# Performance work log

Hardware: AMD Instinct MI355X
Metric: run time of the kernel (lower is better)

## Reference

```python
import jax, jax.numpy as jnp
import numpy as np

DECAY = 0.99
EPS = 1e-05
THRESHOLD = 2.0
CODEBOOK_SIZE = 2048
DIM = 256


def setup_inputs() -> dict:
    key = jax.random.key(0)
    k1, k2, k3 = jax.random.split(key, 3)
    x = jax.random.normal(k1, (32, 1500, DIM), dtype=jnp.float32)
    # kaiming_uniform_ with a=0: bound = sqrt(6 / fan_in)
    bound = float(np.sqrt(6.0 / DIM))
    embed = jax.random.uniform(k2, (CODEBOOK_SIZE, DIM), dtype=jnp.float32,
                               minval=-bound, maxval=bound)
    # warm EMA state: positive cluster sizes, consistent embed_avg
    cluster_size = jax.random.uniform(k3, (CODEBOOK_SIZE,), dtype=jnp.float32,
                                      minval=0.0, maxval=200.0)
    embed_avg = embed * cluster_size[:, None]
    return {"x": x, "embed": embed, "cluster_size": cluster_size,
            "embed_avg": embed_avg}


def reference(x, embed, cluster_size, embed_avg):
    shape = x.shape
    K = embed.shape[0]
    xf = x.reshape(-1, shape[-1])                       # [N, D]

    # quantize: negative squared Euclidean distance, argmax == argmin dist
    x2 = jnp.sum(xf * xf, axis=1, keepdims=True)        # [N, 1]
    e2 = jnp.sum(embed * embed, axis=1)                 # [K]
    dist = -(x2 - 2.0 * (xf @ embed.T) + e2[None, :])   # [N, K]
    embed_ind = jnp.argmax(dist, axis=-1)               # [N]

    # dequantize (embedding gather)
    quantize = embed[embed_ind].reshape(shape)          # [B, T, D]

    # training-path EMA statistics (onehot.sum(0) and x.T @ onehot, as segment sums)
    counts = jax.ops.segment_sum(jnp.ones(xf.shape[0], dtype=x.dtype),
                                 embed_ind, num_segments=K)        # [K]
    embed_sum = jax.ops.segment_sum(xf, embed_ind, num_segments=K) # [K, D]

    new_cluster_size = cluster_size * DECAY + (1.0 - DECAY) * counts
    new_embed_avg = embed_avg * DECAY + (1.0 - DECAY) * embed_sum

    n = new_cluster_size.sum()
    smoothed = (new_cluster_size + EPS) / (n + K * EPS) * n
    embed_normalized = new_embed_avg / smoothed[:, None]

    # dead-code expiration: replace expired codes with random batch vectors
    expired = new_cluster_size < THRESHOLD
    perm = jax.random.permutation(jax.random.key(1), xf.shape[0])[:K]
    replacement = xf[perm]                              # [K, D]
    new_embed = jnp.where(expired[:, None], replacement, embed_normalized)

    codes = embed_ind.reshape(shape[:-1])               # [B, T]
    return quantize, codes, new_cluster_size, new_embed_avg, new_embed
```

## Files before the change

### kernel.cpp

```cpp
#include <hip/hip_runtime.h>
#include <hip/hip_bf16.h>
#include <stdint.h>
#include <math.h>

#define N_TOK 48000
#define DIMS  256
#define KCB   2048
#define WND 0.10f
#define BIAS 32.0f

typedef __attribute__((ext_vector_type(8))) short bf16x8;
typedef __attribute__((ext_vector_type(4))) float f32x4;
typedef __attribute__((ext_vector_type(8))) unsigned short u16x8;

__device__ __forceinline__ unsigned short bf16rn(float f) {
  uint32_t u = __float_as_uint(f);
  uint32_t r = (u + 0x7FFFu + ((u >> 16) & 1u)) >> 16;
  return (unsigned short)r;
}

__device__ __forceinline__ uint32_t packBiased(float fb, uint32_t invIdx) {
  float c = fmaxf(fb, 0.0f);
  return (__float_as_uint(c) & ~0x7FFu) | invIdx;
}
__device__ __forceinline__ uint32_t packThrBiased(float fb) {
  float c = fmaxf(fb, 0.0f);
  return __float_as_uint(c) & ~0x7FFu;
}
__device__ __forceinline__ float unpackBiased(uint32_t u) {
  return __uint_as_float(u & ~0x7FFu);
}
__device__ __forceinline__ void ins3u(uint32_t& b, uint32_t& s, uint32_t& t, uint32_t v) {
  uint32_t lo = min(b, v);
  b = max(b, v);
  uint32_t lo2 = min(s, lo);
  s = max(s, lo);
  t = max(t, lo2);
}

__device__ inline void tf2x32(uint32_t k0, uint32_t k1, uint32_t c0, uint32_t c1,
                              uint32_t& o0, uint32_t& o1) {
  uint32_t ks2 = k0 ^ k1 ^ 0x1BD11BDAu;
  uint32_t x0 = c0 + k0, x1 = c1 + k1;
#define TF_R(r) { x0 += x1; x1 = (x1 << (r)) | (x1 >> (32 - (r))); x1 ^= x0; }
  TF_R(13) TF_R(15) TF_R(26) TF_R(6)
  x0 += k1; x1 += ks2 + 1u;
  TF_R(17) TF_R(29) TF_R(16) TF_R(24)
  x0 += ks2; x1 += k0 + 2u;
  TF_R(13) TF_R(15) TF_R(26) TF_R(6)
  x0 += k0; x1 += k1 + 3u;
  TF_R(17) TF_R(29) TF_R(16) TF_R(24)
  x0 += k1; x1 += ks2 + 4u;
  TF_R(13) TF_R(15) TF_R(26) TF_R(6)
  x0 += ks2; x1 += k0 + 5u;
#undef TF_R
  o0 = x0; o1 = x1;
}

__device__ inline void get_round_key(int round, uint32_t& ka, uint32_t& kb) {
  const uint32_t b0 = 0u, b1 = 1u;
  uint32_t K1a, K1b, S1a, S1b;
  tf2x32(b0, b1, 0u, 0u, K1a, K1b);
  tf2x32(b0, b1, 0u, 1u, S1a, S1b);
  if (round == 1) { ka = S1a; kb = S1b; return; }
  uint32_t S2a, S2b;
  tf2x32(K1a, K1b, 0u, 1u, S2a, S2b);
  ka = S2a; kb = S2b;
}

__device__ inline uint32_t gen_key(int round, uint32_t i) {
  uint32_t ka, kb, o0, o1;
  get_round_key(round, ka, kb);
  tf2x32(ka, kb, 0u, i, o0, o1);
  return o0 ^ o1;
}

__device__ __forceinline__ void gload_lds16(const void* g, void* l) {
  __builtin_amdgcn_global_load_lds(
      (const __attribute__((address_space(1))) uint32_t*)g,
      (__attribute__((address_space(3))) uint32_t*)l, 16, 0, 0);
}

__global__ void e2split(const float* __restrict__ x, unsigned short* __restrict__ xh,
                        const float* __restrict__ embed, unsigned short* __restrict__ eh,
                        float* __restrict__ e2f, double* __restrict__ e2d) {
  const int nx = N_TOK * DIMS / 8;
  const int ne = KCB * DIMS / 8;
  int i = blockIdx.x * blockDim.x + threadIdx.x;
  if (i < nx + ne) {
    const float* src; unsigned short* dst; int j;
    if (i < nx) { src = x; dst = xh; j = i; }
    else { src = embed; dst = eh; j = i - nx; }
    float4 a = ((const float4*)src)[j * 2];
    float4 b = ((const float4*)src)[j * 2 + 1];
    float v[8] = {a.x, a.y, a.z, a.w, b.x, b.y, b.z, b.w};
    u16x8 h;
#pragma unroll
    for (int q = 0; q < 8; ++q) h[q] = bf16rn(v[q]);
    *(u16x8*)&dst[(size_t)j * 8] = h;
    return;
  }
  int k = i - (nx + ne);
  if (k < KCB) {
    const float4* er = (const float4*)(embed + (size_t)k * DIMS);
    float s = 0.f;
    double sd = 0.0;
    for (int c = 0; c < DIMS / 4; ++c) {
      float4 v = er[c];
      s = fmaf(v.x, v.x, s); s = fmaf(v.y, v.y, s);
      s = fmaf(v.z, v.z, s); s = fmaf(v.w, v.w, s);
      sd += (double)v.x * v.x + (double)v.y * v.y
          + (double)v.z * v.z + (double)v.w * v.w;
    }
    e2f[k] = BIAS - s;
    e2d[k] = sd;
  }
}

__global__ __launch_bounds__(256, 2) void dist_mfma(
    const unsigned short* __restrict__ xh, const unsigned short* __restrict__ eh,
    const float* __restrict__ e2f,
    uint32_t* __restrict__ pb, uint32_t* __restrict__ ps, uint32_t* __restrict__ pt)
{
  __shared__ __align__(16) char smem[50688];
  short (*As)[128 * 32] = (short(*)[128 * 32])smem;
  short (*Bs)[256 * 32] = (short(*)[256 * 32])(smem + 16384);
  uint32_t* red = (uint32_t*)smem;

  const int tid = threadIdx.x;
  const int lane = tid & 63, w = tid >> 6;
  const int wr = w >> 1, wc = w & 1;
  const int l15 = lane & 15, lg = lane >> 4;

  int bx, by;
  {
    const int bid = blockIdx.x;
    if (bid < 2944) { int g = bid >> 6, r = bid & 63; bx = g * 8 + (r & 7); by = r >> 3; }
    else            { int t2 = bid - 2944; bx = 368 + (t2 % 7); by = t2 / 7; }
  }
  const int n0 = bx * 128;
  const int c0 = by * 256;

  f32x4 acc[4][8];
#pragma unroll
  for (int mf = 0; mf < 4; ++mf)
#pragma unroll
    for (int nf = 0; nf < 8; ++nf) acc[mf][nf] = (f32x4){0.f, 0.f, 0.f, 0.f};

  auto stage = [&](int t) {
    const int d0 = t << 5;
    const int q = t & 1;
#pragma unroll
    for (int i = 0; i < 2; ++i) {
      const int c = i * 256 + tid;
      const int row = c >> 2;
      const int sc = ((c & 3) ^ ((row >> 1) & 3)) << 3;
      gload_lds16(xh + (size_t)(n0 + row) * DIMS + d0 + sc, (void*)&As[q][c * 8]);
    }
#pragma unroll
    for (int i = 0; i < 4; ++i) {
      const int c = i * 256 + tid;
      const int row = c >> 2;
      const int sc = ((c & 3) ^ ((row >> 1) & 3)) << 3;
      gload_lds16(eh + (size_t)(c0 + row) * DIMS + d0 + sc, (void*)&Bs[q][c * 8]);
    }
  };

  stage(0);
  __syncthreads();

#pragma unroll 1
  for (int t = 0; t < 8; ++t) {
    if (t < 7) stage(t + 1);
    const int q = t & 1;
    bf16x8 af[4], bfv[8];
#pragma unroll
    for (int mf = 0; mf < 4; ++mf) {
      const int r = wr * 64 + mf * 16 + l15;
      af[mf] = *(const bf16x8*)&As[q][r * 32 + ((lg ^ ((r >> 1) & 3)) << 3)];
    }
#pragma unroll
    for (int nf = 0; nf < 8; ++nf) {
      const int r = wc * 128 + nf * 16 + l15;
      bfv[nf] = *(const bf16x8*)&Bs[q][r * 32 + ((lg ^ ((r >> 1) & 3)) << 3)];
    }
#pragma unroll
    for (int mf = 0; mf < 4; ++mf)
#pragma unroll
      for (int nf = 0; nf < 8; ++nf)
        acc[mf][nf] = __builtin_amdgcn_mfma_f32_16x16x32_bf16(
            af[mf], bfv[nf], acc[mf][nf], 0, 0, 0);
    __syncthreads();
  }

  float e2v[8];
  uint32_t inv[8];
#pragma unroll
  for (int nf = 0; nf < 8; ++nf) {
    int k = c0 + wc * 128 + nf * 16 + l15;
    e2v[nf] = e2f[k];
    inv[nf] = 2047u - (uint32_t)k;
  }

  const int colbase = wc * 16 + l15;
#pragma unroll
  for (int mf = 0; mf < 4; ++mf) {
#pragma unroll
    for (int reg = 0; reg < 4; ++reg) {
      uint32_t p0 = packBiased(fmaf(2.f, acc[mf][0][reg], e2v[0]), inv[0]);
      uint32_t p1 = packBiased(fmaf(2.f, acc[mf][1][reg], e2v[1]), inv[1]);
      uint32_t p2 = packBiased(fmaf(2.f, acc[mf][2][reg], e2v[2]), inv[2]);
      uint32_t h1 = max(p0, p1), l1 = min(p0, p1);
      uint32_t b  = max(h1, p2), m  = min(h1, p2);
      uint32_t s  = max(l1, m),  t3 = min(l1, m);
#pragma unroll
      for (int nf = 3; nf < 8; ++nf) {
        float f = fmaf(2.f, acc[mf][nf][reg], e2v[nf]);
        ins3u(b, s, t3, packBiased(f, inv[nf]));
      }
      const int row = wr * 64 + mf * 16 + lg * 4 + reg;
      uint32_t* p = &red[row * 99 + colbase * 3];
      p[0] = b; p[1] = s; p[2] = t3;
    }
  }
  __syncthreads();
  {
    const int row = tid >> 1, half = tid & 1;
    uint32_t b = 0u, s = 0u, t3 = 0u;
    const uint32_t* p = &red[row * 99 + half * 48];
#pragma unroll 4
    for (int c = 0; c < 48; ++c) ins3u(b, s, t3, p[c]);
    if (half) {
      uint32_t* q = &red[row * 99 + 96];
      q[0] = b; q[1] = s; q[2] = t3;
    }
    __syncthreads();
    if (!half) {
      const uint32_t* q = &red[row * 99 + 96];
      ins3u(b, s, t3, q[0]);
      ins3u(b, s, t3, q[1]);
      ins3u(b, s, t3, q[2]);
      size_t o = (size_t)by * N_TOK + n0 + row;
      pb[o] = b; ps[o] = s; pt[o] = t3;
    }
  }
}

__global__ void merge8(const uint32_t* __restrict__ pb, const uint32_t* __restrict__ ps,
                       const uint32_t* __restrict__ pt,
                       int* __restrict__ ind,
                       int* __restrict__ candRows, int* __restrict__ candIdx,
                       int* __restrict__ candCnt, int* __restrict__ listC,
                       uint32_t* __restrict__ cntA, uint32_t* __restrict__ cntC) {
  int n = blockIdx.x * blockDim.x + threadIdx.x;
  if (n >= N_TOK) return;
  uint32_t tb[8], tsv[8], ttv[8];
#pragma unroll
  for (int tt = 0; tt < 8; ++tt) {
    size_t o = (size_t)tt * N_TOK + n;
    tb[tt] = pb[o]; tsv[tt] = ps[o]; ttv[tt] = pt[o];
  }
  uint32_t best = tb[0];
#pragma unroll
  for (int tt = 1; tt < 8; ++tt) best = max(best, tb[tt]);
  ind[n] = 2047 - (int)(best & 0x7FFu);
  const uint32_t thr = packThrBiased(unpackBiased(best) - WND);
  int m = 0; bool full = false;
#pragma unroll
  for (int tt = 0; tt < 8; ++tt) {
    m += (tb[tt] >= thr) + (tsv[tt] >= thr);
    full = full || (ttv[tt] >= thr);
  }
  if (full) {
    listC[atomicAdd(cntC, 1u)] = n;
  } else if (m > 1) {
    uint32_t i = atomicAdd(cntA, 1u);
    candRows[i] = n; candCnt[i] = m;
    int j = 0;
#pragma unroll
    for (int tt = 0; tt < 8; ++tt) {
      if (tb[tt]  >= thr) candIdx[(size_t)i * 16 + (j++)] = 2047 - (int)(tb[tt]  & 0x7FFu);
      if (tsv[tt] >= thr) candIdx[(size_t)i * 16 + (j++)] = 2047 - (int)(tsv[tt] & 0x7FFu);
    }
  }
}

__global__ void refine_cand(const float* __restrict__ x, const float* __restrict__ embed,
                            const double* __restrict__ e2d,
                            const int* __restrict__ candRows, const int* __restrict__ candIdx,
                            const int* __restrict__ candCnt, const uint32_t* __restrict__ cntA,
                            int* __restrict__ ind) {
  const uint32_t nA = cntA[0];
  const int lane = threadIdx.x & 63;
  const uint32_t wid = (blockIdx.x * blockDim.x + threadIdx.x) >> 6;
  const uint32_t nw = (gridDim.x * blockDim.x) >> 6;
  for (uint32_t i = wid; i < nA; i += nw) {
    const int n = candRows[i];
    const int m = candCnt[i];
    float4 xv = ((const float4*)x)[(size_t)n * 64 + lane];
    double best = -1e300; int bk = 0x7fffffff;
    for (int j = 0; j < m; ++j) {
      int k = candIdx[(size_t)i * 16 + j];
      float4 e4 = ((const float4*)embed)[(size_t)k * 64 + lane];
      double d = (double)xv.x * e4.x + (double)xv.y * e4.y
               + (double)xv.z * e4.z + (double)xv.w * e4.w;
#pragma unroll
      for (int mm = 1; mm < 64; mm <<= 1) d += __shfl_xor(d, mm);
      double v = 2.0 * d - e2d[k];
      if (v > best || (v == best && k < bk)) { best = v; bk = k; }
    }
    if (lane == 0) ind[n] = bk;
  }
}

__global__ void refine_fullC(const float* __restrict__ x, const float* __restrict__ embed,
                             const double* __restrict__ e2d,
                             const int* __restrict__ listC, const uint32_t* __restrict__ cntC,
                             int* __restrict__ ind) {
  __shared__ double xd[DIMS];
  __shared__ double rv[256];
  __shared__ int    rk[256];
  const int tid = threadIdx.x;
  const uint32_t nC = cntC[0];
  for (uint32_t it = blockIdx.x; it < nC; it += gridDim.x) {
    const int n = listC[it];
    __syncthreads();
    xd[tid] = (double)x[(size_t)n * DIMS + tid];
    __syncthreads();
    double best = -1e300; int bk = 0x7fffffff;
    for (int k = tid; k < KCB; k += 256) {
      const float4* er = (const float4*)(embed + (size_t)k * DIMS);
      double a0 = 0.0, a1 = 0.0, a2 = 0.0, a3 = 0.0;
      for (int c = 0; c < 64; c += 4) {
        float4 ea = er[c], eb = er[c + 1], ec = er[c + 2], ed = er[c + 3];
        int d = c * 4;
        a0 += xd[d + 0] * ea.x + xd[d + 1] * ea.y + xd[d + 2] * ea.z + xd[d + 3] * ea.w;
        a1 += xd[d + 4] * eb.x + xd[d + 5] * eb.y + xd[d + 6] * eb.z + xd[d + 7] * eb.w;
        a2 += xd[d + 8] * ec.x + xd[d + 9] * ec.y + xd[d + 10] * ec.z + xd[d + 11] * ec.w;
        a3 += xd[d + 12] * ed.x + xd[d + 13] * ed.y + xd[d + 14] * ed.z + xd[d + 15] * ed.w;
      }
      double v = 2.0 * (a0 + a1 + a2 + a3) - e2d[k];
      if (v > best || (v == best && k < bk)) { best = v; bk = k; }
    }
    rv[tid] = best; rk[tid] = bk;
    __syncthreads();
    for (int s = 128; s > 0; s >>= 1) {
      if (tid < s) {
        double v2 = rv[tid + s]; int k2 = rk[tid + s];
        if (v2 > rv[tid] || (v2 == rv[tid] && k2 < rk[tid])) { rv[tid] = v2; rk[tid] = k2; }
      }
      __syncthreads();
    }
    if (tid == 0) ind[n] = rk[0];
  }
}

__global__ void gather_q(const float* __restrict__ embed, const int* __restrict__ ind,
                         float* __restrict__ outq, float* __restrict__ outcodes,
                         uint32_t* __restrict__ cntTok) {
  int idx = blockIdx.x * blockDim.x + threadIdx.x;
  if (idx >= N_TOK * 64) return;
  int n = idx >> 6, c = idx & 63;
  int k = ind[n];
  ((float4*)outq)[idx] = ((const float4*)embed)[(size_t)k * 64 + c];
  if (c == 0) { outcodes[n] = (float)k; atomicAdd(&cntTok[k], 1u); }
}

__global__ void scan_tok_ema(const uint32_t* __restrict__ cntTok, uint32_t* __restrict__ tokBase,
                             uint32_t* __restrict__ tokCur,
                             const float* __restrict__ cs, float* __restrict__ out_ncs,
                             int* __restrict__ expired, double* __restrict__ nsum) {
  __shared__ uint32_t buf[2][2048];
  __shared__ double sd[1024];
  int t = threadIdx.x;
  double local = 0.0;
  for (int q = 0; q < 2; ++q) {
    int i = t + q * 1024;
    uint32_t c = cntTok[i];
    buf[0][i] = c;
    tokCur[i] = 0;
    double v = 0.99 * (double)cs[i] + 0.01 * (double)c;
    out_ncs[i] = (float)v;
    expired[i] = (v < 2.0) ? 1 : 0;
    local += v;
  }
  sd[t] = local;
  __syncthreads();
  int src = 0;
  for (int off = 1; off < 2048; off <<= 1) {
    for (int q = 0; q < 2; ++q) {
      int i = t + q * 1024;
      uint32_t v = buf[src][i];
      if (i >= off) v += buf[src][i - off];
      buf[src ^ 1][i] = v;
    }
    src ^= 1; __syncthreads();
  }
  for (int q = 0; q < 2; ++q) {
    int i = t + q * 1024;
    tokBase[i] = buf[src][i] - cntTok[i];
  }
  for (int s = 512; s > 0; s >>= 1) { if (t < s) sd[t] += sd[t + s]; __syncthreads(); }
  if (t == 0) nsum[0] = sd[0];
}

__global__ void scatter_tok(const int* __restrict__ ind, const uint32_t* __restrict__ tokBase,
                            uint32_t* __restrict__ cursor, uint32_t* __restrict__ tokBucket) {
  int n = blockIdx.x * blockDim.x + threadIdx.x;
  if (n >= N_TOK) return;
  int k = ind[n];
  uint32_t p = atomicAdd(&cursor[k], 1u);
  tokBucket[tokBase[k] + p] = (uint32_t)n;
}

__global__ void esum_bucket(const float* __restrict__ x, const uint32_t* __restrict__ tokBase,
                            const uint32_t* __restrict__ cntTok,
                            const uint32_t* __restrict__ tokBucket,
                            float* __restrict__ esum) {
  const uint32_t wv = (blockIdx.x * blockDim.x + threadIdx.x) >> 6;
  if (wv >= KCB) return;
  const int lane = threadIdx.x & 63;
  const uint32_t base = tokBase[wv], cnt = cntTok[wv];
  float4 a0 = {0.f, 0.f, 0.f, 0.f}, a1 = {0.f, 0.f, 0.f, 0.f};
  uint32_t i = 0;
  for (; i + 2 <= cnt; i += 2) {
    uint32_t n0 = tokBucket[base + i], n1 = tokBucket[base + i + 1];
    float4 v0 = ((const float4*)x)[(size_t)n0 * 64 + lane];
    float4 v1 = ((const float4*)x)[(size_t)n1 * 64 + lane];
    a0.x += v0.x; a0.y += v0.y; a0.z += v0.z; a0.w += v0.w;
    a1.x += v1.x; a1.y += v1.y; a1.z += v1.z; a1.w += v1.w;
  }
  if (i < cnt) {
    uint32_t n0 = tokBucket[base + i];
    float4 v0 = ((const float4*)x)[(size_t)n0 * 64 + lane];
    a0.x += v0.x; a0.y += v0.y; a0.z += v0.z; a0.w += v0.w;
  }
  float4 r; r.x = a0.x + a1.x; r.y = a0.y + a1.y; r.z = a0.z + a1.z; r.w = a0.w + a1.w;
  ((float4*)esum)[(size_t)wv * 64 + lane] = r;
}

__global__ void final_embed(const float* __restrict__ x, const float* __restrict__ cs,
                            const uint32_t* __restrict__ cntTok,
                            const float* __restrict__ eavg, const float* __restrict__ esum,
                            const int* __restrict__ expired, const double* __restrict__ nsum,
                            const uint32_t* __restrict__ perm,
                            float* __restrict__ out_eavg, float* __restrict__ out_ne) {
  int idx = blockIdx.x * blockDim.x + threadIdx.x;
  if (idx >= KCB * 64) return;
  int k = idx >> 6, c = idx & 63;
  float4 ea = ((const float4*)eavg)[idx];
  float4 es = ((const float4*)esum)[idx];
  double ax = 0.99 * (double)ea.x + 0.01 * (double)es.x;
  double ay = 0.99 * (double)ea.y + 0.01 * (double)es.y;
  double az = 0.99 * (double)ea.z + 0.01 * (double)es.z;
  double aw = 0.99 * (double)ea.w + 0.01 * (double)es.w;
  float4 nv; nv.x = (float)ax; nv.y = (float)ay; nv.z = (float)az; nv.w = (float)aw;
  ((float4*)out_eavg)[idx] = nv;
  float4 r;
  if (expired[k]) {
    r = ((const float4*)x)[(size_t)perm[k] * 64 + c];
  } else {
    double ncs = 0.99 * (double)cs[k] + 0.01 * (double)cntTok[k];
    double n = nsum[0];
    double sm = (ncs + 1e-5) / (n + 2048.0 * 1e-5) * n;
    r.x = (float)(ax / sm); r.y = (float)(ay / sm);
    r.z = (float)(az / sm); r.w = (float)(aw / sm);
  }
  ((float4*)out_ne)[idx] = r;
}

__global__ void keys_both(uint32_t* __restrict__ keys1, uint32_t* __restrict__ keys2,
                          uint32_t* __restrict__ bcount1, uint32_t* __restrict__ bcount2) {
  int i = blockIdx.x * blockDim.x + threadIdx.x;
  if (i >= N_TOK) return;
  uint32_t k1 = gen_key(1, (uint32_t)i);
  uint32_t k2 = gen_key(2, (uint32_t)i);
  keys1[i] = k1; keys2[i] = k2;
  atomicAdd(&bcount1[k1 >> 21], 1u);
  atomicAdd(&bcount2[k2 >> 21], 1u);
}

__global__ void scan_both(const uint32_t* __restrict__ in1, uint32_t* __restrict__ out1,
                          uint32_t* __restrict__ cur1,
                          const uint32_t* __restrict__ in2, uint32_t* __restrict__ out2,
                          uint32_t* __restrict__ cur2) {
  const uint32_t* in = blockIdx.x ? in2 : in1;
  uint32_t* out = blockIdx.x ? out2 : out1;
  uint32_t* cz = blockIdx.x ? cur2 : cur1;
  __shared__ uint32_t buf[2][2048];
  int t = threadIdx.x;
  for (int q = 0; q < 2; ++q) buf[0][t + q * 1024] = in[t + q * 1024];
  cz[t] = 0; cz[t + 1024] = 0;
  __syncthreads();
  int src = 0;
  for (int off = 1; off < 2048; off <<= 1) {
    for (int q = 0; q < 2; ++q) {
      int i = t + q * 1024;
      uint32_t v = buf[src][i];
      if (i >= off) v += buf[src][i - off];
      buf[src ^ 1][i] = v;
    }
    src ^= 1; __syncthreads();
  }
  for (int q = 0; q < 2; ++q) {
    int i = t + q * 1024;
    out[i] = buf[src][i] - in[i];
  }
}

__global__ void scatter1(const uint32_t* __restrict__ keys1, const uint32_t* __restrict__ bbase1,
                         uint32_t* __restrict__ cursor1,
                         uint32_t* __restrict__ bkey, uint32_t* __restrict__ bval) {
  int i = blockIdx.x * blockDim.x + threadIdx.x;
  if (i >= N_TOK) return;
  uint32_t k = keys1[i];
  uint32_t b = k >> 21;
  uint32_t p = atomicAdd(&cursor1[b], 1u);
  uint32_t s = bbase1[b] + p;
  bkey[s] = k; bval[s] = (uint32_t)i;
}

__global__ void rank1_scatter2(const uint32_t* __restrict__ bkey, const uint32_t* __restrict__ bval,
                               const uint32_t* __restrict__ bbase1, const uint32_t* __restrict__ bcount1,
                               const uint32_t* __restrict__ keys2,
                               const uint32_t* __restrict__ bbase2, uint32_t* __restrict__ cursor2,
                               uint32_t* __restrict__ bkey2, uint32_t* __restrict__ bval2,
                               uint32_t* __restrict__ bpos2) {
  int b = blockIdx.x;
  uint32_t base = bbase1[b], cnt = bcount1[b];
  for (uint32_t t = threadIdx.x; t < cnt; t += blockDim.x) {
    uint32_t k = bkey[base + t], pv = bval[base + t];
    uint32_t r = 0;
    for (uint32_t j = 0; j < cnt; ++j) {
      uint32_t kj = bkey[base + j], pj = bval[base + j];
      r += (kj < k) | ((kj == k) & (pj < pv));
    }
    uint32_t p = base + r;
    uint32_t k2 = keys2[p];
    uint32_t b2 = k2 >> 21;
    uint32_t q = atomicAdd(&cursor2[b2], 1u);
    uint32_t s = bbase2[b2] + q;
    bkey2[s] = k2; bval2[s] = pv; bpos2[s] = p;
  }
}

__global__ void rank2(const uint32_t* __restrict__ bkey2, const uint32_t* __restrict__ bval2,
                      const uint32_t* __restrict__ bpos2,
                      const uint32_t* __restrict__ bbase2, const uint32_t* __restrict__ bcount2,
                      uint32_t* __restrict__ perm) {
  int b = blockIdx.x;
  uint32_t base = bbase2[b];
  if (base >= KCB) return;
  uint32_t cnt = bcount2[b];
  for (uint32_t t = threadIdx.x; t < cnt; t += blockDim.x) {
    uint32_t k = bkey2[base + t], p = bpos2[base + t];
    uint32_t r = 0;
    for (uint32_t j = 0; j < cnt; ++j) {
      uint32_t kj = bkey2[base + j], pj = bpos2[base + j];
      r += (kj < k) | ((kj == k) & (pj < p));
    }
    uint32_t pos = base + r;
    if (pos < KCB) perm[pos] = bval2[base + t];
  }
}

extern "C" void kernel_launch(void* const* d_in, const int* in_sizes, int n_in,
                              void* d_out, int out_size, void* d_ws, size_t ws_size,
                              hipStream_t stream) {
  const float* x     = (const float*)d_in[0];
  const float* embed = (const float*)d_in[1];
  const float* cs    = (const float*)d_in[2];
  const float* eavg  = (const float*)d_in[3];

  float* out = (float*)d_out;
  float* outQ    = out;
  float* outC    = out + 12288000;
  float* outNCS  = out + 12336000;
  float* outEAVG = out + 12338048;
  float* outNE   = out + 12862336;

  char* w = (char*)d_ws;
  size_t off = 0;
  auto alloc = [&](size_t bytes) -> void* {
    void* p = w + off; off += (bytes + 255) & ~(size_t)255; return p;
  };
  unsigned short* xh = (unsigned short*)alloc((size_t)N_TOK * DIMS * 2);
  unsigned short* eh = (unsigned short*)alloc((size_t)KCB * DIMS * 2);
  float*    e2f     = (float*)alloc(KCB * 4);
  double*   e2d     = (double*)alloc(KCB * 8);
  float*    esum    = (float*)alloc((size_t)KCB * DIMS * 4);
  uint32_t* pbest   = (uint32_t*)alloc((size_t)8 * N_TOK * 4);
  uint32_t* psecond = (uint32_t*)alloc((size_t)8 * N_TOK * 4);
  uint32_t* pthird  = (uint32_t*)alloc((size_t)8 * N_TOK * 4);
  int*      ind     = (int*)alloc(N_TOK * 4);
  int*      candRows= (int*)alloc(N_TOK * 4);
  int*      candCnt = (int*)alloc(N_TOK * 4);
  int*      candIdx = (int*)alloc((size_t)N_TOK * 16 * 4);
  int*      listC   = (int*)alloc(N_TOK * 4);
  double*   nsum    = (double*)alloc(256);
  int*      expired = (int*)alloc(KCB * 4);
  uint32_t* tokBase = (uint32_t*)alloc(KCB * 4);
  uint32_t* tokCur  = (uint32_t*)alloc(KCB * 4);
  uint32_t* tokBucket = (uint32_t*)alloc(N_TOK * 4);
  uint32_t* keys1   = (uint32_t*)alloc(N_TOK * 4);
  uint32_t* keys2   = (uint32_t*)alloc(N_TOK * 4);
  uint32_t* bkey    = (uint32_t*)alloc(N_TOK * 4);
  uint32_t* bval    = (uint32_t*)alloc(N_TOK * 4);
  uint32_t* bkey2   = (uint32_t*)alloc(N_TOK * 4);
  uint32_t* bval2   = (uint32_t*)alloc(N_TOK * 4);
  uint32_t* bpos2   = (uint32_t*)alloc(N_TOK * 4);
  uint32_t* bbase1  = (uint32_t*)alloc(KCB * 4);
  uint32_t* bbase2  = (uint32_t*)alloc(KCB * 4);
  uint32_t* cursor1 = (uint32_t*)alloc(KCB * 4);
  uint32_t* cursor2 = (uint32_t*)alloc(KCB * 4);
  uint32_t* perm    = (uint32_t*)alloc(KCB * 4);
  uint32_t* cntAB   = (uint32_t*)alloc(256);
  uint32_t* cntTok  = (uint32_t*)alloc(KCB * 4);
  uint32_t* bcount1 = (uint32_t*)alloc(KCB * 4);
  uint32_t* bcount2 = (uint32_t*)alloc(KCB * 4);

  hipMemsetAsync(cntAB, 0, 256 + 3 * KCB * 4, stream);

  e2split<<<(N_TOK * DIMS / 8 + KCB * DIMS / 8 + KCB + 255) / 256, 256, 0, stream>>>(
      x, xh, embed, eh, e2f, e2d);

  keys_both<<<188, 256, 0, stream>>>(keys1, keys2, bcount1, bcount2);
  scan_both<<<2, 1024, 0, stream>>>(bcount1, bbase1, cursor1, bcount2, bbase2, cursor2);

  dist_mfma<<<3000, 256, 0, stream>>>(xh, eh, e2f, pbest, psecond, pthird);
  merge8<<<188, 256, 0, stream>>>(pbest, psecond, pthird,
                                  ind, candRows, candIdx, candCnt, listC,
                                  &cntAB[0], &cntAB[1]);
  refine_cand<<<512, 256, 0, stream>>>(x, embed, e2d, candRows, candIdx, candCnt,
                                       &cntAB[0], ind);
  refine_fullC<<<1024, 256, 0, stream>>>(x, embed, e2d, listC, &cntAB[1], ind);

  gather_q<<<12000, 256, 0, stream>>>(embed, ind, outQ, outC, cntTok);
  scan_tok_ema<<<1, 1024, 0, stream>>>(cntTok, tokBase, tokCur, cs, outNCS, expired, nsum);
  scatter_tok<<<188, 256, 0, stream>>>(ind, tokBase, tokCur, tokBucket);
  esum_bucket<<<512, 256, 0, stream>>>(x, tokBase, cntTok, tokBucket, esum);

  scatter1<<<188, 256, 0, stream>>>(keys1, bbase1, cursor1, bkey, bval);
  rank1_scatter2<<<2048, 64, 0, stream>>>(bkey, bval, bbase1, bcount1,
                                          keys2, bbase2, cursor2, bkey2, bval2, bpos2);
  rank2<<<2048, 64, 0, stream>>>(bkey2, bval2, bpos2, bbase2, bcount2, perm);

  final_embed<<<512, 256, 0, stream>>>(x, cs, cntTok, eavg, esum, expired, nsum,
                                       perm, outEAVG, outNE);
}
```

Baseline: 260.7 us.

## Merge independent small kernels to cut launch count and serialization

Independent stages are folded into shared launches: key generation goes into the bf16 split kernel, the two refine kernels become one grid partitioned by block index, the three prefix scans run as one 3-block kernel, and the token and key scatters are combined. The permutation rank1 stage also runs alongside the esum gather. This removes roughly five kernel launches and the gaps between dependent small launches. The cost is more heterogeneous blocks inside a launch, and rank1 now uses 256-thread blocks where it used 64 threads.

```diff
diff --git a/kernel.cpp b/kernel.cpp
--- a/kernel.cpp
+++ b/kernel.cpp
@@ -81,9 +81,11 @@
       (__attribute__((address_space(3))) uint32_t*)l, 16, 0, 0);
 }
 
-__global__ void e2split(const float* __restrict__ x, unsigned short* __restrict__ xh,
-                        const float* __restrict__ embed, unsigned short* __restrict__ eh,
-                        float* __restrict__ e2f, double* __restrict__ e2d) {
+__global__ void e2split_keys(const float* __restrict__ x, unsigned short* __restrict__ xh,
+                             const float* __restrict__ embed, unsigned short* __restrict__ eh,
+                             float* __restrict__ e2f, double* __restrict__ e2d,
+                             uint32_t* __restrict__ keys1, uint32_t* __restrict__ keys2,
+                             uint32_t* __restrict__ bcount1, uint32_t* __restrict__ bcount2) {
   const int nx = N_TOK * DIMS / 8;
   const int ne = KCB * DIMS / 8;
   int i = blockIdx.x * blockDim.x + threadIdx.x;
@@ -114,6 +116,15 @@
     }
     e2f[k] = BIAS - s;
     e2d[k] = sd;
+    return;
+  }
+  int n = k - KCB;
+  if (n < N_TOK) {
+    uint32_t k1 = gen_key(1, (uint32_t)n);
+    uint32_t k2 = gen_key(2, (uint32_t)n);
+    keys1[n] = k1; keys2[n] = k2;
+    atomicAdd(&bcount1[k1 >> 21], 1u);
+    atomicAdd(&bcount2[k2 >> 21], 1u);
   }
 }
 
@@ -285,44 +296,45 @@
   }
 }
 
-__global__ void refine_cand(const float* __restrict__ x, const float* __restrict__ embed,
+#define RC_BLOCKS 512
+#define RF_BLOCKS 1024
+__global__ void refine_both(const float* __restrict__ x, const float* __restrict__ embed,
                             const double* __restrict__ e2d,
                             const int* __restrict__ candRows, const int* __restrict__ candIdx,
-                            const int* __restrict__ candCnt, const uint32_t* __restrict__ cntA,
+                            const int* __restrict__ candCnt,
+                            const int* __restrict__ listC,
+                            const uint32_t* __restrict__ cntAB,
                             int* __restrict__ ind) {
-  const uint32_t nA = cntA[0];
-  const int lane = threadIdx.x & 63;
-  const uint32_t wid = (blockIdx.x * blockDim.x + threadIdx.x) >> 6;
-  const uint32_t nw = (gridDim.x * blockDim.x) >> 6;
-  for (uint32_t i = wid; i < nA; i += nw) {
-    const int n = candRows[i];
-    const int m = candCnt[i];
-    float4 xv = ((const float4*)x)[(size_t)n * 64 + lane];
-    double best = -1e300; int bk = 0x7fffffff;
-    for (int j = 0; j < m; ++j) {
-      int k = candIdx[(size_t)i * 16 + j];
-      float4 e4 = ((const float4*)embed)[(size_t)k * 64 + lane];
-      double d = (double)xv.x * e4.x + (double)xv.y * e4.y
-               + (double)xv.z * e4.z + (double)xv.w * e4.w;
-#pragma unroll
-      for (int mm = 1; mm < 64; mm <<= 1) d += __shfl_xor(d, mm);
-      double v = 2.0 * d - e2d[k];
-      if (v > best || (v == best && k < bk)) { best = v; bk = k; }
-    }
-    if (lane == 0) ind[n] = bk;
-  }
-}
-
-__global__ void refine_fullC(const float* __restrict__ x, const float* __restrict__ embed,
-                             const double* __restrict__ e2d,
-                             const int* __restrict__ listC, const uint32_t* __restrict__ cntC,
-                             int* __restrict__ ind) {
   __shared__ double xd[DIMS];
   __shared__ double rv[256];
   __shared__ int    rk[256];
   const int tid = threadIdx.x;
-  const uint32_t nC = cntC[0];
-  for (uint32_t it = blockIdx.x; it < nC; it += gridDim.x) {
+  if (blockIdx.x < RC_BLOCKS) {
+    const uint32_t nA = cntAB[0];
+    const int lane = tid & 63;
+    const uint32_t wid = ((uint32_t)blockIdx.x * 256 + tid) >> 6;
+    const uint32_t nw = RC_BLOCKS * 4;
+    for (uint32_t i = wid; i < nA; i += nw) {
+      const int n = candRows[i];
+      const int m = candCnt[i];
+      float4 xv = ((const float4*)x)[(size_t)n * 64 + lane];
+      double best = -1e300; int bk = 0x7fffffff;
+      for (int j = 0; j < m; ++j) {
+        int k = candIdx[(size_t)i * 16 + j];
+        float4 e4 = ((const float4*)embed)[(size_t)k * 64 + lane];
+        double d = (double)xv.x * e4.x + (double)xv.y * e4.y
+                 + (double)xv.z * e4.z + (double)xv.w * e4.w;
+#pragma unroll
+        for (int mm = 1; mm < 64; mm <<= 1) d += __shfl_xor(d, mm);
+        double v = 2.0 * d - e2d[k];
+        if (v > best || (v == best && k < bk)) { best = v; bk = k; }
+      }
+      if (lane == 0) ind[n] = bk;
+    }
+    return;
+  }
+  const uint32_t nC = cntAB[1];
+  for (uint32_t it = blockIdx.x - RC_BLOCKS; it < nC; it += RF_BLOCKS) {
     const int n = listC[it];
     __syncthreads();
     xd[tid] = (double)x[(size_t)n * DIMS + tid];
@@ -366,25 +378,35 @@
   if (c == 0) { outcodes[n] = (float)k; atomicAdd(&cntTok[k], 1u); }
 }
 
-__global__ void scan_tok_ema(const uint32_t* __restrict__ cntTok, uint32_t* __restrict__ tokBase,
-                             uint32_t* __restrict__ tokCur,
-                             const float* __restrict__ cs, float* __restrict__ out_ncs,
-                             int* __restrict__ expired, double* __restrict__ nsum) {
+__global__ void scan3(const uint32_t* __restrict__ cntTok, uint32_t* __restrict__ tokBase,
+                      uint32_t* __restrict__ tokCur,
+                      const float* __restrict__ cs, float* __restrict__ out_ncs,
+                      int* __restrict__ expired, double* __restrict__ nsum,
+                      const uint32_t* __restrict__ bcount1, uint32_t* __restrict__ bbase1,
+                      uint32_t* __restrict__ cursor1,
+                      const uint32_t* __restrict__ bcount2, uint32_t* __restrict__ bbase2,
+                      uint32_t* __restrict__ cursor2) {
   __shared__ uint32_t buf[2][2048];
   __shared__ double sd[1024];
   int t = threadIdx.x;
+  const uint32_t* in; uint32_t* out; uint32_t* cz;
+  if (blockIdx.x == 0)      { in = cntTok;  out = tokBase; cz = tokCur;  }
+  else if (blockIdx.x == 1) { in = bcount1; out = bbase1;  cz = cursor1; }
+  else                      { in = bcount2; out = bbase2;  cz = cursor2; }
   double local = 0.0;
   for (int q = 0; q < 2; ++q) {
     int i = t + q * 1024;
-    uint32_t c = cntTok[i];
+    uint32_t c = in[i];
     buf[0][i] = c;
-    tokCur[i] = 0;
-    double v = 0.99 * (double)cs[i] + 0.01 * (double)c;
-    out_ncs[i] = (float)v;
-    expired[i] = (v < 2.0) ? 1 : 0;
-    local += v;
-  }
-  sd[t] = local;
+    cz[i] = 0;
+    if (blockIdx.x == 0) {
+      double v = 0.99 * (double)cs[i] + 0.01 * (double)c;
+      out_ncs[i] = (float)v;
+      expired[i] = (v < 2.0) ? 1 : 0;
+      local += v;
+    }
+  }
+  if (blockIdx.x == 0) sd[t] = local;
   __syncthreads();
   int src = 0;
   for (int off = 1; off < 2048; off <<= 1) {
@@ -398,45 +420,101 @@
   }
   for (int q = 0; q < 2; ++q) {
     int i = t + q * 1024;
-    tokBase[i] = buf[src][i] - cntTok[i];
-  }
-  for (int s = 512; s > 0; s >>= 1) { if (t < s) sd[t] += sd[t + s]; __syncthreads(); }
-  if (t == 0) nsum[0] = sd[0];
-}
-
-__global__ void scatter_tok(const int* __restrict__ ind, const uint32_t* __restrict__ tokBase,
-                            uint32_t* __restrict__ cursor, uint32_t* __restrict__ tokBucket) {
+    out[i] = buf[src][i] - in[i];
+  }
+  if (blockIdx.x == 0) {
+    for (int s = 512; s > 0; s >>= 1) { if (t < s) sd[t] += sd[t + s]; __syncthreads(); }
+    if (t == 0) nsum[0] = sd[0];
+  }
+}
+
+__global__ void scatter_both(const int* __restrict__ ind, const uint32_t* __restrict__ tokBase,
+                             uint32_t* __restrict__ tokCur, uint32_t* __restrict__ tokBucket,
+                             const uint32_t* __restrict__ keys1, const uint32_t* __restrict__ bbase1,
+                             uint32_t* __restrict__ cursor1,
+                             uint32_t* __restrict__ bkey, uint32_t* __restrict__ bval) {
   int n = blockIdx.x * blockDim.x + threadIdx.x;
   if (n >= N_TOK) return;
   int k = ind[n];
-  uint32_t p = atomicAdd(&cursor[k], 1u);
+  uint32_t p = atomicAdd(&tokCur[k], 1u);
   tokBucket[tokBase[k] + p] = (uint32_t)n;
-}
-
-__global__ void esum_bucket(const float* __restrict__ x, const uint32_t* __restrict__ tokBase,
-                            const uint32_t* __restrict__ cntTok,
-                            const uint32_t* __restrict__ tokBucket,
-                            float* __restrict__ esum) {
-  const uint32_t wv = (blockIdx.x * blockDim.x + threadIdx.x) >> 6;
-  if (wv >= KCB) return;
-  const int lane = threadIdx.x & 63;
-  const uint32_t base = tokBase[wv], cnt = cntTok[wv];
-  float4 a0 = {0.f, 0.f, 0.f, 0.f}, a1 = {0.f, 0.f, 0.f, 0.f};
-  uint32_t i = 0;
-  for (; i + 2 <= cnt; i += 2) {
-    uint32_t n0 = tokBucket[base + i], n1 = tokBucket[base + i + 1];
-    float4 v0 = ((const float4*)x)[(size_t)n0 * 64 + lane];
-    float4 v1 = ((const float4*)x)[(size_t)n1 * 64 + lane];
-    a0.x += v0.x; a0.y += v0.y; a0.z += v0.z; a0.w += v0.w;
-    a1.x += v1.x; a1.y += v1.y; a1.z += v1.z; a1.w += v1.w;
-  }
-  if (i < cnt) {
-    uint32_t n0 = tokBucket[base + i];
-    float4 v0 = ((const float4*)x)[(size_t)n0 * 64 + lane];
-    a0.x += v0.x; a0.y += v0.y; a0.z += v0.z; a0.w += v0.w;
-  }
-  float4 r; r.x = a0.x + a1.x; r.y = a0.y + a1.y; r.z = a0.z + a1.z; r.w = a0.w + a1.w;
-  ((float4*)esum)[(size_t)wv * 64 + lane] = r;
+  uint32_t k1 = keys1[n];
+  uint32_t b = k1 >> 21;
+  uint32_t q = atomicAdd(&cursor1[b], 1u);
+  uint32_t s = bbase1[b] + q;
+  bkey[s] = k1; bval[s] = (uint32_t)n;
+}
+
+#define ES_BLOCKS 512
+__global__ void esum_rank1(const float* __restrict__ x, const uint32_t* __restrict__ tokBase,
+                           const uint32_t* __restrict__ cntTok,
+                           const uint32_t* __restrict__ tokBucket,
+                           float* __restrict__ esum,
+                           const uint32_t* __restrict__ bkey, const uint32_t* __restrict__ bval,
+                           const uint32_t* __restrict__ bbase1, const uint32_t* __restrict__ bcount1,
+                           const uint32_t* __restrict__ keys2,
+                           const uint32_t* __restrict__ bbase2, uint32_t* __restrict__ cursor2,
+                           uint32_t* __restrict__ bkey2, uint32_t* __restrict__ bval2,
+                           uint32_t* __restrict__ bpos2) {
+  const int tid = threadIdx.x;
+  if (blockIdx.x < ES_BLOCKS) {
+    const uint32_t wv = ((uint32_t)blockIdx.x * 256 + tid) >> 6;
+    const int lane = tid & 63;
+    const uint32_t base = tokBase[wv], cnt = cntTok[wv];
+    float4 a0 = {0.f, 0.f, 0.f, 0.f}, a1 = {0.f, 0.f, 0.f, 0.f};
+    uint32_t i = 0;
+    for (; i + 2 <= cnt; i += 2) {
+      uint32_t n0 = tokBucket[base + i], n1 = tokBucket[base + i + 1];
+      float4 v0 = ((const float4*)x)[(size_t)n0 * 64 + lane];
+      float4 v1 = ((const float4*)x)[(size_t)n1 * 64 + lane];
+      a0.x += v0.x; a0.y += v0.y; a0.z += v0.z; a0.w += v0.w;
+      a1.x += v1.x; a1.y += v1.y; a1.z += v1.z; a1.w += v1.w;
+    }
+    if (i < cnt) {
+      uint32_t n0 = tokBucket[base + i];
+      float4 v0 = ((const float4*)x)[(size_t)n0 * 64 + lane];
+      a0.x += v0.x; a0.y += v0.y; a0.z += v0.z; a0.w += v0.w;
+    }
+    float4 r; r.x = a0.x + a1.x; r.y = a0.y + a1.y; r.z = a0.z + a1.z; r.w = a0.w + a1.w;
+    ((float4*)esum)[(size_t)wv * 64 + lane] = r;
+    return;
+  }
+  int b = blockIdx.x - ES_BLOCKS;
+  uint32_t base = bbase1[b], cnt = bcount1[b];
+  for (uint32_t t = tid; t < cnt; t += 256) {
+    uint32_t k = bkey[base + t], pv = bval[base + t];
+    uint32_t r = 0;
+    for (uint32_t j = 0; j < cnt; ++j) {
+      uint32_t kj = bkey[base + j], pj = bval[base + j];
+      r += (kj < k) | ((kj == k) & (pj < pv));
+    }
+    uint32_t p = base + r;
+    uint32_t k2 = keys2[p];
+    uint32_t b2 = k2 >> 21;
+    uint32_t q = atomicAdd(&cursor2[b2], 1u);
+    uint32_t s = bbase2[b2] + q;
+    bkey2[s] = k2; bval2[s] = pv; bpos2[s] = p;
+  }
+}
+
+__global__ void rank2(const uint32_t* __restrict__ bkey2, const uint32_t* __restrict__ bval2,
+                      const uint32_t* __restrict__ bpos2,
+                      const uint32_t* __restrict__ bbase2, const uint32_t* __restrict__ bcount2,
+                      uint32_t* __restrict__ perm) {
+  int b = blockIdx.x;
+  uint32_t base = bbase2[b];
+  if (base >= KCB) return;
+  uint32_t cnt = bcount2[b];
+  for (uint32_t t = threadIdx.x; t < cnt; t += blockDim.x) {
+    uint32_t k = bkey2[base + t], p = bpos2[base + t];
+    uint32_t r = 0;
+    for (uint32_t j = 0; j < cnt; ++j) {
+      uint32_t kj = bkey2[base + j], pj = bpos2[base + j];
+      r += (kj < k) | ((kj == k) & (pj < p));
+    }
+    uint32_t pos = base + r;
+    if (pos < KCB) perm[pos] = bval2[base + t];
+  }
 }
 
 __global__ void final_embed(const float* __restrict__ x, const float* __restrict__ cs,
@@ -467,101 +545,6 @@
     r.z = (float)(az / sm); r.w = (float)(aw / sm);
   }
   ((float4*)out_ne)[idx] = r;
-}
-
-__global__ void keys_both(uint32_t* __restrict__ keys1, uint32_t* __restrict__ keys2,
-                          uint32_t* __restrict__ bcount1, uint32_t* __restrict__ bcount2) {
-  int i = blockIdx.x * blockDim.x + threadIdx.x;
-  if (i >= N_TOK) return;
-  uint32_t k1 = gen_key(1, (uint32_t)i);
-  uint32_t k2 = gen_key(2, (uint32_t)i);
-  keys1[i] = k1; keys2[i] = k2;
-  atomicAdd(&bcount1[k1 >> 21], 1u);
-  atomicAdd(&bcount2[k2 >> 21], 1u);
-}
-
-__global__ void scan_both(const uint32_t* __restrict__ in1, uint32_t* __restrict__ out1,
-                          uint32_t* __restrict__ cur1,
-                          const uint32_t* __restrict__ in2, uint32_t* __restrict__ out2,
-                          uint32_t* __restrict__ cur2) {
-  const uint32_t* in = blockIdx.x ? in2 : in1;
-  uint32_t* out = blockIdx.x ? out2 : out1;
-  uint32_t* cz = blockIdx.x ? cur2 : cur1;
-  __shared__ uint32_t buf[2][2048];
-  int t = threadIdx.x;
-  for (int q = 0; q < 2; ++q) buf[0][t + q * 1024] = in[t + q * 1024];
-  cz[t] = 0; cz[t + 1024] = 0;
-  __syncthreads();
-  int src = 0;
-  for (int off = 1; off < 2048; off <<= 1) {
-    for (int q = 0; q < 2; ++q) {
-      int i = t + q * 1024;
-      uint32_t v = buf[src][i];
-      if (i >= off) v += buf[src][i - off];
-      buf[src ^ 1][i] = v;
-    }
-    src ^= 1; __syncthreads();
-  }
-  for (int q = 0; q < 2; ++q) {
-    int i = t + q * 1024;
-    out[i] = buf[src][i] - in[i];
-  }
-}
-
-__global__ void scatter1(const uint32_t* __restrict__ keys1, const uint32_t* __restrict__ bbase1,
-                         uint32_t* __restrict__ cursor1,
-                         uint32_t* __restrict__ bkey, uint32_t* __restrict__ bval) {
-  int i = blockIdx.x * blockDim.x + threadIdx.x;
-  if (i >= N_TOK) return;
-  uint32_t k = keys1[i];
-  uint32_t b = k >> 21;
-  uint32_t p = atomicAdd(&cursor1[b], 1u);
-  uint32_t s = bbase1[b] + p;
-  bkey[s] = k; bval[s] = (uint32_t)i;
-}
-
-__global__ void rank1_scatter2(const uint32_t* __restrict__ bkey, const uint32_t* __restrict__ bval,
-                               const uint32_t* __restrict__ bbase1, const uint32_t* __restrict__ bcount1,
-                               const uint32_t* __restrict__ keys2,
-                               const uint32_t* __restrict__ bbase2, uint32_t* __restrict__ cursor2,
-                               uint32_t* __restrict__ bkey2, uint32_t* __restrict__ bval2,
-                               uint32_t* __restrict__ bpos2) {
-  int b = blockIdx.x;
-  uint32_t base = bbase1[b], cnt = bcount1[b];
-  for (uint32_t t = threadIdx.x; t < cnt; t += blockDim.x) {
-    uint32_t k = bkey[base + t], pv = bval[base + t];
-    uint32_t r = 0;
-    for (uint32_t j = 0; j < cnt; ++j) {
-      uint32_t kj = bkey[base + j], pj = bval[base + j];
-      r += (kj < k) | ((kj == k) & (pj < pv));
-    }
-    uint32_t p = base + r;
-    uint32_t k2 = keys2[p];
-    uint32_t b2 = k2 >> 21;
-    uint32_t q = atomicAdd(&cursor2[b2], 1u);
-    uint32_t s = bbase2[b2] + q;
-    bkey2[s] = k2; bval2[s] = pv; bpos2[s] = p;
-  }
-}
-
-__global__ void rank2(const uint32_t* __restrict__ bkey2, const uint32_t* __restrict__ bval2,
-                      const uint32_t* __restrict__ bpos2,
-                      const uint32_t* __restrict__ bbase2, const uint32_t* __restrict__ bcount2,
-                      uint32_t* __restrict__ perm) {
-  int b = blockIdx.x;
-  uint32_t base = bbase2[b];
-  if (base >= KCB) return;
-  uint32_t cnt = bcount2[b];
-  for (uint32_t t = threadIdx.x; t < cnt; t += blockDim.x) {
-    uint32_t k = bkey2[base + t], p = bpos2[base + t];
-    uint32_t r = 0;
-    for (uint32_t j = 0; j < cnt; ++j) {
-      uint32_t kj = bkey2[base + j], pj = bpos2[base + j];
-      r += (kj < k) | ((kj == k) & (pj < p));
-    }
-    uint32_t pos = base + r;
-    if (pos < KCB) perm[pos] = bval2[base + t];
-  }
 }
 
 extern "C" void kernel_launch(void* const* d_in, const int* in_sizes, int n_in,
@@ -621,28 +604,24 @@
 
   hipMemsetAsync(cntAB, 0, 256 + 3 * KCB * 4, stream);
 
-  e2split<<<(N_TOK * DIMS / 8 + KCB * DIMS / 8 + KCB + 255) / 256, 256, 0, stream>>>(
-      x, xh, embed, eh, e2f, e2d);
-
-  keys_both<<<188, 256, 0, stream>>>(keys1, keys2, bcount1, bcount2);
-  scan_both<<<2, 1024, 0, stream>>>(bcount1, bbase1, cursor1, bcount2, bbase2, cursor2);
+  e2split_keys<<<(N_TOK * DIMS / 8 + KCB * DIMS / 8 + KCB + N_TOK + 255) / 256, 256, 0,
+                 stream>>>(x, xh, embed, eh, e2f, e2d, keys1, keys2, bcount1, bcount2);
 
   dist_mfma<<<3000, 256, 0, stream>>>(xh, eh, e2f, pbest, psecond, pthird);
   merge8<<<188, 256, 0, stream>>>(pbest, psecond, pthird,
                                   ind, candRows, candIdx, candCnt, listC,
                                   &cntAB[0], &cntAB[1]);
-  refine_cand<<<512, 256, 0, stream>>>(x, embed, e2d, candRows, candIdx, candCnt,
-                                       &cntAB[0], ind);
-  refine_fullC<<<1024, 256, 0, stream>>>(x, embed, e2d, listC, &cntAB[1], ind);
+  refine_both<<<RC_BLOCKS + RF_BLOCKS, 256, 0, stream>>>(
+      x, embed, e2d, candRows, candIdx, candCnt, listC, cntAB, ind);
 
   gather_q<<<12000, 256, 0, stream>>>(embed, ind, outQ, outC, cntTok);
-  scan_tok_ema<<<1, 1024, 0, stream>>>(cntTok, tokBase, tokCur, cs, outNCS, expired, nsum);
-  scatter_tok<<<188, 256, 0, stream>>>(ind, tokBase, tokCur, tokBucket);
-  esum_bucket<<<512, 256, 0, stream>>>(x, tokBase, cntTok, tokBucket, esum);
-
-  scatter1<<<188, 256, 0, stream>>>(keys1, bbase1, cursor1, bkey, bval);
-  rank1_scatter2<<<2048, 64, 0, stream>>>(bkey, bval, bbase1, bcount1,
-                                          keys2, bbase2, cursor2, bkey2, bval2, bpos2);
+  scan3<<<3, 1024, 0, stream>>>(cntTok, tokBase, tokCur, cs, outNCS, expired, nsum,
+                                bcount1, bbase1, cursor1, bcount2, bbase2, cursor2);
+  scatter_both<<<188, 256, 0, stream>>>(ind, tokBase, tokCur, tokBucket,
+                                        keys1, bbase1, cursor1, bkey, bval);
+  esum_rank1<<<ES_BLOCKS + KCB, 256, 0, stream>>>(
+      x, tokBase, cntTok, tokBucket, esum,
+      bkey, bval, bbase1, bcount1, keys2, bbase2, cursor2, bkey2, bval2, bpos2);
   rank2<<<2048, 64, 0, stream>>>(bkey2, bval2, bpos2, bbase2, bcount2, perm);
 
   final_embed<<<512, 256, 0, stream>>>(x, cs, cntTok, eavg, esum, expired, nsum,
```

Measured after the change: 235.5 us. 9.6% less time.
